# Kernel tuning notes

Hardware: AMD Instinct MI355X
Metric: run time of the kernel (lower is better)

The kernel has to match this reference:

```python
import jax, jax.numpy as jnp
import numpy as np

KSIZE, STRIDE, H, W = 7, 4, 128, 128
NH = (H - KSIZE) // STRIDE + 1  # 31
L = NH * NH                     # 961 patches


def conv2d(x, w, b=None, stride=1):
    y = jax.lax.conv_general_dilated(x, w, (stride, stride), 'VALID',
                                     dimension_numbers=('NCHW', 'OIHW', 'NCHW'))
    if b is not None:
        y = y + b[None, :, None, None]
    return y


def refpad(x):
    return jnp.pad(x, ((0, 0), (0, 0), (1, 1), (1, 1)), mode='reflect')


def unfold(x, k, s):
    # torch.nn.Unfold equivalent, returned as (B, C, k, k, L)
    B, C, Hh, Ww = x.shape
    nh = (Hh - k) // s + 1
    nw = (Ww - k) // s + 1
    hi = (jnp.arange(nh) * s)[:, None] + jnp.arange(k)  # (nh, k)
    wi = (jnp.arange(nw) * s)[:, None] + jnp.arange(k)  # (nw, k)
    p = x[:, :, hi]            # (B, C, nh, k, W)
    p = p[:, :, :, :, wi]      # (B, C, nh, k, nw, k)
    p = p.transpose(0, 1, 3, 5, 2, 4).reshape(B, C, k, k, nh * nw)
    return p


def fold(patches, Hh, Ww, k, s):
    # patches: (B, nh, nw, C, k, k); overlap-add like torch.nn.functional.fold
    B, nh, nw, C = patches.shape[0], patches.shape[1], patches.shape[2], patches.shape[3]
    hi = (jnp.arange(nh) * s)[:, None] + jnp.arange(k)  # (nh, k)
    wi = (jnp.arange(nw) * s)[:, None] + jnp.arange(k)  # (nw, k)
    H_idx = hi[:, None, :, None]  # (nh, 1, k, 1)
    W_idx = wi[None, :, None, :]  # (1, nw, 1, k)
    vals = patches.transpose(0, 3, 1, 2, 4, 5)  # (B, C, nh, nw, k, k)
    out = jnp.zeros((B, C, Hh, Ww), patches.dtype)
    return out.at[:, :, H_idx, W_idx].add(vals)


def setup_inputs() -> dict:
    key = jax.random.key(0)
    ks = jax.random.split(key, 16)
    Cin, Ci = 32, 16            # in_channels, inter_channels
    F_in = KSIZE * KSIZE * Ci   # 784
    F_out = F_in // 4           # 196
    s = 0.05
    d = {
        'x':       jax.random.normal(ks[0], (8, Cin, H, W), jnp.float32),
        'g_w':     jax.random.normal(ks[1], (Ci, Cin, 3, 3), jnp.float32) * s,
        'g_b':     jax.random.normal(ks[2], (Ci,), jnp.float32) * s,
        'w_w':     jax.random.normal(ks[3], (Ci, Cin, 3, 3), jnp.float32) * s,
        'w_b':     jax.random.normal(ks[4], (Ci,), jnp.float32) * s,
        'theta_w': jax.random.normal(ks[5], (Cin, Ci, 1, 1), jnp.float32) * s,
        'theta_b': jax.random.normal(ks[6], (Cin,), jnp.float32) * s,
        'fc1_w':   jax.random.normal(ks[7], (F_out, F_in), jnp.float32) * s,
        'fc1_b':   jax.random.normal(ks[8], (F_out,), jnp.float32) * s,
        'mconv_w': jax.random.normal(ks[9], (L, L), jnp.float32) * s,
        'mconv_b': jax.random.normal(ks[10], (L,), jnp.float32) * s,
        'mfc_w':   jax.random.normal(ks[11], (L, L), jnp.float32) * s,
        'mfc_b':   jax.random.normal(ks[12], (L,), jnp.float32) * s,
        'c1_w':    jax.random.normal(ks[13], (Cin // 2, Cin, 3, 3), jnp.float32) * s,
        'c2_w':    jax.random.normal(ks[14], (Cin, Cin // 2, 1, 1), jnp.float32) * s,
    }
    return d


def reference(x, g_w, g_b, w_w, w_b, theta_w, theta_b, fc1_w, fc1_b,
              mconv_w, mconv_b, mfc_w, mfc_b, c1_w, c2_w):
    residual = x
    x1 = conv2d(refpad(x), g_w, g_b)        # (B, Ci, H, W)
    x2 = conv2d(refpad(x), w_w, w_b)        # (B, Ci, H, W)
    x3 = conv2d(x1, theta_w, theta_b)       # (B, Cin, H, W)
    B = x.shape[0]
    Cin = x.shape[1]

    p6 = unfold(x1, KSIZE, STRIDE).transpose(0, 4, 1, 2, 3).reshape(B, L, -1)   # (B,L,Ci*49)
    p4 = unfold(x2, KSIZE, STRIDE).transpose(0, 4, 1, 2, 3).reshape(B, L, -1)   # (B,L,Ci*49)
    p62 = unfold(x3, KSIZE, STRIDE).transpose(0, 4, 1, 2, 3).reshape(B, L, -1)  # (B,L,Cin*49)

    wf = p4 @ fc1_w.T + fc1_b   # (B, L, F)
    xf = p6 @ fc1_w.T + fc1_b   # (B, L, F)
    A = jnp.einsum('blf,bmf->blm', wf, xf)  # (B, L, L)

    # Ti1 (Conv1d k=1 over patch dim) + Ti2 (Linear over patch dim, transposed)
    Ti = jnp.einsum('nc,bcm->bnm', mconv_w + mfc_w, A) + (mconv_b + mfc_b)[None, :, None]
    mask = jax.nn.sigmoid(Ti)
    mask_b = (mask != 0.0).astype(A.dtype)

    scale = wf.shape[-1] ** -0.5
    Am = jax.nn.softmax(A * mask * scale, axis=-1) * mask_b  # (B, L, L)

    y = jnp.einsum('blm,bmf->blf', Am, p62)  # (B, L, Cin*49)
    y = y.reshape(B, NH, NH, Cin, KSIZE, KSIZE)
    out = fold(y, H, W, KSIZE, STRIDE)       # (B, Cin, H, W)

    # BasicBlock: conv3x3(reflect) -> lrelu -> conv1x1 -> lrelu
    o = jax.nn.leaky_relu(conv2d(refpad(out), c1_w), 0.2)
    o = jax.nn.leaky_relu(conv2d(o, c2_w), 0.2)
    out = residual + o
    return Am, out
```

## Files before the change

kernel.cpp:

```cpp
#include <hip/hip_runtime.h>
#include <math.h>

namespace {
constexpr int Bn   = 8;
constexpr int CIN  = 32;
constexpr int CI   = 16;
constexpr int Lp   = 961;
constexpr int FIN  = 784;
constexpr int FOUT = 196;
constexpr int F62  = 1568;

constexpr int FCP  = 224;
constexpr long long FCB = 961LL * FCP;
constexpr int KP   = 992;
constexpr long long WFTB = 196LL * KP;
constexpr long long AMBB = 961LL * KP;
constexpr long long PBTB = 1568LL * KP;
constexpr long long AB   = 961LL * 961;
constexpr int YLD  = 964;
constexpr long long YB = 1568LL * YLD;
}

typedef __attribute__((ext_vector_type(8))) short short8x;
typedef __attribute__((ext_vector_type(4))) float floatx4;
typedef __attribute__((ext_vector_type(4))) unsigned short ushort4x;

static __device__ __forceinline__ unsigned short f2bf(float x) {
    unsigned int u = __builtin_bit_cast(unsigned int, x);
    u += 0x7fffu + ((u >> 16) & 1u);
    return (unsigned short)(u >> 16);
}
static __device__ __forceinline__ float bf2f(unsigned short h) {
    return __builtin_bit_cast(float, ((unsigned int)h) << 16);
}

__global__ __launch_bounds__(256)
void prep_k(const float* __restrict__ g_w, const float* __restrict__ w_w,
            const float* __restrict__ c1_w,
            float* __restrict__ wT1, float* __restrict__ wT2,
            float* __restrict__ wTc,
            const float* __restrict__ mconv_w, const float* __restrict__ mfc_w,
            unsigned short* __restrict__ Mwh, unsigned short* __restrict__ Mwl,
            const float* __restrict__ mconv_b, const float* __restrict__ mfc_b,
            float* __restrict__ Mb,
            const float* __restrict__ fc1w,
            unsigned short* __restrict__ Wh, unsigned short* __restrict__ Wl,
            unsigned short* __restrict__ wfTh, unsigned short* __restrict__ wfTl)
{
    int i = blockIdx.x * 256 + threadIdx.x;
    if (i < 13824) {
        int sel = i / 4608, r = i - sel * 4608;
        int tapidx = r >> 4, co = r & 15;
        const float* w = (sel == 0) ? g_w : (sel == 1) ? w_w : c1_w;
        float* t = (sel == 0) ? wT1 : (sel == 1) ? wT2 : wTc;
        t[r] = w[co * 288 + tapidx];
    } else if (i < 967136) {
        int k = i - 13824;
        int n = k / KP, c = k - n * KP;
        float v = (c < 961) ? (mconv_w[n * 961 + c] + mfc_w[n * 961 + c]) : 0.0f;
        unsigned short h = f2bf(v);
        Mwh[k] = h; Mwl[k] = f2bf(v - bf2f(h));
    } else if (i < 968097) {
        int k = i - 967136;
        Mb[k] = mconv_b[k] + mfc_b[k];
    } else if (i < 1172897) {
        int k = i - 968097;
        int n = k / 800, kk = k - n * 800;
        float v = (n < 196 && kk < 784) ? fc1w[n * 784 + kk] : 0.0f;
        unsigned short h = f2bf(v);
        Wh[k] = h; Wl[k] = f2bf(v - bf2f(h));
    } else if (i < 1223073) {
        int k = i - 1172897;
        int row = k >> 5, c = k & 31;
        long long pos = (long long)row * KP + 960 + c;
        wfTh[pos] = 0; wfTl[pos] = 0;
    }
}

template<bool DUAL, bool BIAS, bool LEAKY>
__global__ __launch_bounds__(256)
void conv3x3t_k(const float* __restrict__ x,
                const float* __restrict__ wT1, const float* __restrict__ b1,
                const float* __restrict__ wT2, const float* __restrict__ b2,
                float* __restrict__ o1, float* __restrict__ o2)
{
    __shared__ float Ls[10880];
    const int tid = threadIdx.x;
    const int t  = blockIdx.x;
    const int wt = t & 3, ht = (t >> 2) & 15, b = t >> 6;
    const int h0 = ht * 8, w0 = wt * 32;
    const float* xb = x + (size_t)b * CIN * 16384;

    for (int i = tid; i < 10880; i += 256) {
        int ci  = i / 340;
        int rem = i - ci * 340;
        int row = rem / 34;
        int col = rem - row * 34;
        int gh = h0 + row - 1; gh = (gh < 0) ? 1 : (gh > 127 ? 126 : gh);
        int gw = w0 + col - 1; gw = (gw < 0) ? 1 : (gw > 127 ? 126 : gw);
        Ls[i] = xb[ci * 16384 + gh * 128 + gw];
    }
    __syncthreads();

    const int px = tid & 31, py = tid >> 5;
    float acc1[16], acc2[16];
    #pragma unroll
    for (int co = 0; co < 16; ++co) {
        acc1[co] = BIAS ? b1[co] : 0.0f;
        acc2[co] = (DUAL && BIAS) ? b2[co] : 0.0f;
    }

    for (int ci = 0; ci < 32; ++ci) {
        const float* lp = &Ls[ci * 340 + py * 34 + px];
        float vv[9];
        #pragma unroll
        for (int r = 0; r < 3; ++r)
            #pragma unroll
            for (int c = 0; c < 3; ++c)
                vv[r * 3 + c] = lp[r * 34 + c];
        const float* wr1 = wT1 + ci * 144;
        const float* wr2 = DUAL ? (wT2 + ci * 144) : nullptr;
        #pragma unroll
        for (int tp = 0; tp < 9; ++tp) {
            float v = vv[tp];
            #pragma unroll
            for (int co = 0; co < 16; ++co) {
                acc1[co] += v * wr1[tp * 16 + co];
                if constexpr (DUAL) acc2[co] += v * wr2[tp * 16 + co];
            }
        }
    }

    const int h = h0 + py, w = w0 + px;
    size_t ob = (((size_t)b * 16) * 128 + h) * 128 + w;
    #pragma unroll
    for (int co = 0; co < 16; ++co) {
        float v = acc1[co];
        if constexpr (LEAKY) v = (v >= 0.0f) ? v : 0.2f * v;
        o1[ob + (size_t)co * 16384] = v;
        if constexpr (DUAL) o2[ob + (size_t)co * 16384] = acc2[co];
    }
}

template<bool BIAS, bool LEAKY, bool RESID>
__global__ __launch_bounds__(256)
void conv1x1p_k(const float* __restrict__ src, const float* __restrict__ wgt,
                const float* __restrict__ bias, const float* __restrict__ resid,
                float* __restrict__ out)
{
    int idx = blockIdx.x * 256 + threadIdx.x;
    int pix = idx & 16383;
    int b   = idx >> 14;
    const float* sb = src + (size_t)b * CI * 16384 + pix;
    float s[16];
    #pragma unroll
    for (int ci = 0; ci < CI; ++ci) s[ci] = sb[ci * 16384];
    size_t ob = (size_t)b * 32 * 16384 + pix;
    #pragma unroll
    for (int co = 0; co < 32; ++co) {
        const float* wrow = wgt + co * CI;
        float acc = BIAS ? bias[co] : 0.0f;
        #pragma unroll
        for (int ci = 0; ci < CI; ++ci) acc += wrow[ci] * s[ci];
        if constexpr (LEAKY) acc = (acc >= 0.0f) ? acc : 0.2f * acc;
        if constexpr (RESID) acc += resid[ob + (size_t)co * 16384];
        out[ob + (size_t)co * 16384] = acc;
    }
}

template<bool WRT>
__global__ __launch_bounds__(256)
void fcmfma_k(const float* __restrict__ xsrc,
              const unsigned short* __restrict__ Wh,
              const unsigned short* __restrict__ Wl,
              const float* __restrict__ bias,
              unsigned short* __restrict__ Dh, unsigned short* __restrict__ Dl,
              unsigned short* __restrict__ DTh, unsigned short* __restrict__ DTl)
{
    __shared__ unsigned short AsH[64*32], AsL[64*32], BsH[64*32], BsL[64*32];
    const int tid = threadIdx.x;
    const int tm0 = (blockIdx.x >> 2) * 64;
    const int tn0 = (blockIdx.x & 3) * 64;

    const int lr = tid >> 2;
    const int lc = tid & 3;
    const int gm = tm0 + lr;
    const bool mok = gm < 7688;
    int gbase = 0;
    if (mok) {
        int b = gm / 961, pi = gm - b * 961;
        int ih = pi / 31, iw = pi - ih * 31;
        gbase = b * 262144 + ih * 512 + iw * 4;
    }
    const int pc = ((lc ^ ((lr >> 1) & 3))) * 8;
    const unsigned short* Whr = Wh + (tn0 + lr) * 800;
    const unsigned short* Wlr = Wl + (tn0 + lr) * 800;

    const int lane = tid & 63, wv = tid >> 6;
    const int wm = (wv >> 1) * 32, wn = (wv & 1) * 32;
    const int fr = lane & 15, kq = lane >> 4;

    floatx4 acc[2][2];
    #pragma unroll
    for (int i = 0; i < 2; ++i)
        #pragma unroll
        for (int j = 0; j < 2; ++j)
            acc[i][j] = (floatx4){0.f, 0.f, 0.f, 0.f};

    float pv[8];
    short8x pwh, pwl;
    auto loadA = [&](int k0) {
        #pragma unroll
        for (int j = 0; j < 8; ++j) {
            int k = k0 + lc * 8 + j;
            float v = 0.0f;
            if (mok && k < 784) {
                int c  = k / 49, r = k - c * 49;
                int kh = r / 7,  kw = r - kh * 7;
                v = xsrc[gbase + c * 16384 + kh * 128 + kw];
            }
            pv[j] = v;
        }
    };
    auto loadW = [&](int k0) {
        pwh = *(const short8x*)(Whr + k0 + lc * 8);
        pwl = *(const short8x*)(Wlr + k0 + lc * 8);
    };

    loadA(0); loadW(0);
    for (int k0 = 0; k0 < 800; k0 += 32) {
        unsigned short hv[8], lv[8];
        #pragma unroll
        for (int j = 0; j < 8; ++j) {
            unsigned short h = f2bf(pv[j]);
            hv[j] = h; lv[j] = f2bf(pv[j] - bf2f(h));
        }
        *(short8x*)&AsH[lr * 32 + pc] = *(short8x*)hv;
        *(short8x*)&AsL[lr * 32 + pc] = *(short8x*)lv;
        *(short8x*)&BsH[lr * 32 + pc] = pwh;
        *(short8x*)&BsL[lr * 32 + pc] = pwl;
        __syncthreads();
        if (k0 + 32 < 800) { loadA(k0 + 32); loadW(k0 + 32); }
        short8x ah[2], al[2], bh[2], bl[2];
        #pragma unroll
        for (int i = 0; i < 2; ++i) {
            int mr = wm + i * 16 + fr;
            int off = mr * 32 + ((kq ^ ((mr >> 1) & 3)) * 8);
            ah[i] = *(const short8x*)&AsH[off];
            al[i] = *(const short8x*)&AsL[off];
        }
        #pragma unroll
        for (int j = 0; j < 2; ++j) {
            int nr = wn + j * 16 + fr;
            int off = nr * 32 + ((kq ^ ((nr >> 1) & 3)) * 8);
            bh[j] = *(const short8x*)&BsH[off];
            bl[j] = *(const short8x*)&BsL[off];
        }
        #pragma unroll
        for (int i = 0; i < 2; ++i)
            #pragma unroll
            for (int j = 0; j < 2; ++j) {
                acc[i][j] = __builtin_amdgcn_mfma_f32_16x16x32_bf16(ah[i], bh[j], acc[i][j], 0, 0, 0);
                acc[i][j] = __builtin_amdgcn_mfma_f32_16x16x32_bf16(ah[i], bl[j], acc[i][j], 0, 0, 0);
                acc[i][j] = __builtin_amdgcn_mfma_f32_16x16x32_bf16(al[i], bh[j], acc[i][j], 0, 0, 0);
            }
        __syncthreads();
    }

    #pragma unroll
    for (int j = 0; j < 2; ++j) {
        int n = tn0 + wn + j * 16 + fr;
        if (n >= FCP) continue;
        float bn = (n < 196) ? bias[n] : 0.0f;
        #pragma unroll
        for (int i = 0; i < 2; ++i) {
            #pragma unroll
            for (int r = 0; r < 4; ++r) {
                int l = tm0 + wm + i * 16 + kq * 4 + r;
                if (l >= 7688) continue;
                int b = l / 961, pi = l - b * 961;
                float v = (n < 196) ? (acc[i][j][r] + bn) : 0.0f;
                unsigned short h = f2bf(v);
                unsigned short lo = f2bf(v - bf2f(h));
                long long base = (long long)b * FCB + (long long)pi * FCP + n;
                Dh[base] = h;
                Dl[base] = lo;
                if constexpr (WRT) {
                    if (n < 196) {
                        long long tb = (long long)b * WFTB + (long long)n * KP + pi;
                        DTh[tb] = h;
                        DTl[tb] = lo;
                    }
                }
            }
        }
    }
}

__global__ __launch_bounds__(256)
void w2mfma_k(const unsigned short* __restrict__ Xhi,
              const unsigned short* __restrict__ Xlo,
              const unsigned short* __restrict__ Yhi,
              const unsigned short* __restrict__ Ylo,
              unsigned short* __restrict__ W2h,
              unsigned short* __restrict__ W2l)
{
    __shared__ unsigned short XsH[4096], XsL[4096], YsH[4096], YsL[4096];
    const int b   = blockIdx.x & 7;
    const int t   = blockIdx.x >> 3;
    const int tm0 = (t >> 1) * 128;
    const int tn0 = (t & 1) * 128;
    const unsigned short* Ybh = Yhi + (long long)b * WFTB;
    const unsigned short* Ybl = Ylo + (long long)b * WFTB;
    const int tid = threadIdx.x;

    const int sr  = tid >> 1;
    const int sc0 = (tid & 1) * 2;
    const bool xok = (tm0 + sr) < 961;
    const bool yok = (tn0 + sr) < 196;
    const unsigned short* Xrh = Xhi + (long long)(tm0 + sr) * KP;
    const unsigned short* Xrl = Xlo + (long long)(tm0 + sr) * KP;
    const unsigned short* Yrh = Ybh + (long long)(tn0 + sr) * KP;
    const unsigned short* Yrl = Ybl + (long long)(tn0 + sr) * KP;
    const int swz = (sr >> 1) & 3;

    const int lane = tid & 63;
    const int wv   = tid >> 6;
    const int wm   = (wv >> 1) * 64, wn = (wv & 1) * 64;
    const int fr   = lane & 15;
    const int kq   = lane >> 4;

    floatx4 acc[4][4];
    #pragma unroll
    for (int i = 0; i < 4; ++i)
        #pragma unroll
        for (int j = 0; j < 4; ++j)
            acc[i][j] = (floatx4){0.f, 0.f, 0.f, 0.f};

    const short8x zz = {0,0,0,0,0,0,0,0};
    short8x pxh[2], pxl[2], pyh[2], pyl[2];
    auto loadK = [&](int k0) {
        #pragma unroll
        for (int c = 0; c < 2; ++c) {
            int kc = sc0 + c;
            pxh[c] = xok ? *(const short8x*)(Xrh + k0 + kc * 8) : zz;
            pxl[c] = xok ? *(const short8x*)(Xrl + k0 + kc * 8) : zz;
            pyh[c] = yok ? *(const short8x*)(Yrh + k0 + kc * 8) : zz;
            pyl[c] = yok ? *(const short8x*)(Yrl + k0 + kc * 8) : zz;
        }
    };

    loadK(0);
    for (int k0 = 0; k0 < KP; k0 += 32) {
        #pragma unroll
        for (int c = 0; c < 2; ++c) {
            int pc = (sc0 + c) ^ swz;
            *(short8x*)&XsH[sr * 32 + pc * 8] = pxh[c];
            *(short8x*)&XsL[sr * 32 + pc * 8] = pxl[c];
            *(short8x*)&YsH[sr * 32 + pc * 8] = pyh[c];
            *(short8x*)&YsL[sr * 32 + pc * 8] = pyl[c];
        }
        __syncthreads();
        if (k0 + 32 < KP) loadK(k0 + 32);
        short8x bh[4], bl[4];
        #pragma unroll
        for (int j = 0; j < 4; ++j) {
            int nr = wn + j * 16 + fr;
            int off = nr * 32 + ((kq ^ ((nr >> 1) & 3)) * 8);
            bh[j] = *(const short8x*)&YsH[off];
            bl[j] = *(const short8x*)&YsL[off];
        }
        #pragma unroll
        for (int i = 0; i < 4; ++i) {
            int mr = wm + i * 16 + fr;
            int off = mr * 32 + ((kq ^ ((mr >> 1) & 3)) * 8);
            short8x ah = *(const short8x*)&XsH[off];
            short8x al = *(const short8x*)&XsL[off];
            #pragma unroll
            for (int j = 0; j < 4; ++j) {
                acc[i][j] = __builtin_amdgcn_mfma_f32_16x16x32_bf16(ah, bh[j], acc[i][j], 0, 0, 0);
                acc[i][j] = __builtin_amdgcn_mfma_f32_16x16x32_bf16(ah, bl[j], acc[i][j], 0, 0, 0);
                acc[i][j] = __builtin_amdgcn_mfma_f32_16x16x32_bf16(al, bh[j], acc[i][j], 0, 0, 0);
            }
        }
        __syncthreads();
    }

    unsigned short* Wh2 = W2h + (long long)b * FCB;
    unsigned short* Wl2 = W2l + (long long)b * FCB;
    #pragma unroll
    for (int j = 0; j < 4; ++j) {
        int f = tn0 + wn + j * 16 + fr;
        if (f >= FCP) continue;
        #pragma unroll
        for (int i = 0; i < 4; ++i) {
            int lb = tm0 + wm + i * 16 + kq * 4;
            #pragma unroll
            for (int r = 0; r < 4; ++r) {
                int l = lb + r;
                if (l >= 961) continue;
                float v = acc[i][j][r];
                unsigned short h = f2bf(v);
                long long pos = (long long)l * FCP + f;
                Wh2[pos] = h;
                Wl2[pos] = f2bf(v - bf2f(h));
            }
        }
    }
}

__global__ __launch_bounds__(256)
void atimfma_k(const unsigned short* __restrict__ Wfh,
               const unsigned short* __restrict__ Wfl,
               const unsigned short* __restrict__ W2h,
               const unsigned short* __restrict__ W2l,
               const unsigned short* __restrict__ Xfh,
               const unsigned short* __restrict__ Xfl,
               const float* __restrict__ Mb,
               float* __restrict__ Sout)
{
    __shared__ unsigned short smem[24576];
    unsigned short* X1H = smem;
    unsigned short* X1L = smem + 4096;
    unsigned short* X2H = smem + 8192;
    unsigned short* X2L = smem + 12288;
    unsigned short* YH  = smem + 16384;
    unsigned short* YL  = smem + 20480;

    const int b   = blockIdx.x & 7;
    const int t   = blockIdx.x >> 3;
    const int tm0 = (t >> 3) * 128;
    const int tn0 = (t & 7) * 128;
    const int tid = threadIdx.x;

    const int sr  = tid >> 1;
    const int sc0 = (tid & 1) * 2;
    const bool xok = (tm0 + sr) < 961;
    const bool yok = (tn0 + sr) < 961;
    const unsigned short* X1rh = Wfh + (long long)b * FCB + (long long)(tm0 + sr) * FCP;
    const unsigned short* X1rl = Wfl + (long long)b * FCB + (long long)(tm0 + sr) * FCP;
    const unsigned short* X2rh = W2h + (long long)b * FCB + (long long)(tm0 + sr) * FCP;
    const unsigned short* X2rl = W2l + (long long)b * FCB + (long long)(tm0 + sr) * FCP;
    const unsigned short* Yrh  = Xfh + (long long)b * FCB + (long long)(tn0 + sr) * FCP;
    const unsigned short* Yrl  = Xfl + (long long)b * FCB + (long long)(tn0 + sr) * FCP;
    const int swz = (sr >> 1) & 3;

    const int lane = tid & 63;
    const int wv   = tid >> 6;
    const int wm   = (wv >> 1) * 64, wn = (wv & 1) * 64;
    const int fr   = lane & 15;
    const int kq   = lane >> 4;

    floatx4 accA[4][4], accT[4][4];
    #pragma unroll
    for (int i = 0; i < 4; ++i)
        #pragma unroll
        for (int j = 0; j < 4; ++j) {
            accA[i][j] = (floatx4){0.f, 0.f, 0.f, 0.f};
            accT[i][j] = (floatx4){0.f, 0.f, 0.f, 0.f};
        }

    const short8x zz = {0,0,0,0,0,0,0,0};
    short8x p1h[2], p1l[2], p2h[2], p2l[2], pyh[2], pyl[2];
    auto loadK = [&](int k0) {
        #pragma unroll
        for (int c = 0; c < 2; ++c) {
            int kc = sc0 + c;
            p1h[c] = xok ? *(const short8x*)(X1rh + k0 + kc * 8) : zz;
            p1l[c] = xok ? *(const short8x*)(X1rl + k0 + kc * 8) : zz;
            p2h[c] = xok ? *(const short8x*)(X2rh + k0 + kc * 8) : zz;
            p2l[c] = xok ? *(const short8x*)(X2rl + k0 + kc * 8) : zz;
            pyh[c] = yok ? *(const short8x*)(Yrh  + k0 + kc * 8) : zz;
            pyl[c] = yok ? *(const short8x*)(Yrl  + k0 + kc * 8) : zz;
        }
    };

    loadK(0);
    for (int k0 = 0; k0 < FCP; k0 += 32) {
        #pragma unroll
        for (int c = 0; c < 2; ++c) {
            int pc = (sc0 + c) ^ swz;
            *(short8x*)&X1H[sr * 32 + pc * 8] = p1h[c];
            *(short8x*)&X1L[sr * 32 + pc * 8] = p1l[c];
            *(short8x*)&X2H[sr * 32 + pc * 8] = p2h[c];
            *(short8x*)&X2L[sr * 32 + pc * 8] = p2l[c];
            *(short8x*)&YH[sr * 32 + pc * 8]  = pyh[c];
            *(short8x*)&YL[sr * 32 + pc * 8]  = pyl[c];
        }
        __syncthreads();
        if (k0 + 32 < FCP) loadK(k0 + 32);
        short8x bh[4], bl[4];
        #pragma unroll
        for (int j = 0; j < 4; ++j) {
            int nr = wn + j * 16 + fr;
            int off = nr * 32 + ((kq ^ ((nr >> 1) & 3)) * 8);
            bh[j] = *(const short8x*)&YH[off];
            bl[j] = *(const short8x*)&YL[off];
        }
        #pragma unroll
        for (int i = 0; i < 4; ++i) {
            int mr = wm + i * 16 + fr;
            int off = mr * 32 + ((kq ^ ((mr >> 1) & 3)) * 8);
            short8x a1h = *(const short8x*)&X1H[off];
            short8x a1l = *(const short8x*)&X1L[off];
            short8x a2h = *(const short8x*)&X2H[off];
            short8x a2l = *(const short8x*)&X2L[off];
            #pragma unroll
            for (int j = 0; j < 4; ++j) {
                accA[i][j] = __builtin_amdgcn_mfma_f32_16x16x32_bf16(a1h, bh[j], accA[i][j], 0, 0, 0);
                accA[i][j] = __builtin_amdgcn_mfma_f32_16x16x32_bf16(a1h, bl[j], accA[i][j], 0, 0, 0);
                accA[i][j] = __builtin_amdgcn_mfma_f32_16x16x32_bf16(a1l, bh[j], accA[i][j], 0, 0, 0);
                accT[i][j] = __builtin_amdgcn_mfma_f32_16x16x32_bf16(a2h, bh[j], accT[i][j], 0, 0, 0);
                accT[i][j] = __builtin_amdgcn_mfma_f32_16x16x32_bf16(a2h, bl[j], accT[i][j], 0, 0, 0);
                accT[i][j] = __builtin_amdgcn_mfma_f32_16x16x32_bf16(a2l, bh[j], accT[i][j], 0, 0, 0);
            }
        }
        __syncthreads();
    }

    const float scale = 0.07142857142857142f;
    float* Sb = Sout + (long long)b * AB;
    #pragma unroll
    for (int j = 0; j < 4; ++j) {
        int m = tn0 + wn + j * 16 + fr;
        if (m >= 961) continue;
        #pragma unroll
        for (int i = 0; i < 4; ++i) {
            int lb = tm0 + wm + i * 16 + kq * 4;
            #pragma unroll
            for (int r = 0; r < 4; ++r) {
                int l = lb + r;
                if (l >= 961) continue;
                float ti = accT[i][j][r] + Mb[l];
                float mask = 1.0f / (1.0f + expf(-ti));
                Sb[(long long)l * 961 + m] = accA[i][j][r] * mask * scale;
            }
        }
    }
}

__global__ __launch_bounds__(256)
void softmax_mask_k(const float* __restrict__ S, float* __restrict__ Am,
                    unsigned short* __restrict__ Amb)
{
    int row = blockIdx.x;
    const float* srow = S + (long long)row * Lp;
    float*       orow = Am + (long long)row * Lp;
    unsigned short* brow = Amb + (long long)row * KP;
    int tid = threadIdx.x;

    float s[4], mb[4];
    float lmax = -INFINITY;
    #pragma unroll
    for (int j = 0; j < 4; ++j) {
        int m = tid + j * 256;
        if (m < Lp) {
            float v = srow[m];
            s[j]  = v;
            mb[j] = (v != 0.0f) ? 1.0f : 0.0f;
            lmax  = fmaxf(lmax, v);
        } else { s[j] = -INFINITY; mb[j] = 0.0f; }
    }
    __shared__ float red[256];
    red[tid] = lmax; __syncthreads();
    #pragma unroll
    for (int off = 128; off > 0; off >>= 1) {
        if (tid < off) red[tid] = fmaxf(red[tid], red[tid + off]);
        __syncthreads();
    }
    float rmax = red[0];
    __syncthreads();

    float e[4];
    float lsum = 0.0f;
    #pragma unroll
    for (int j = 0; j < 4; ++j) {
        int m = tid + j * 256;
        e[j] = (m < Lp) ? expf(s[j] - rmax) : 0.0f;
        lsum += e[j];
    }
    red[tid] = lsum; __syncthreads();
    #pragma unroll
    for (int off = 128; off > 0; off >>= 1) {
        if (tid < off) red[tid] += red[tid + off];
        __syncthreads();
    }
    float inv = 1.0f / red[0];
    #pragma unroll
    for (int j = 0; j < 4; ++j) {
        int m = tid + j * 256;
        if (m < Lp) {
            float v = e[j] * inv * mb[j];
            orow[m] = v;
            brow[m] = f2bf(v);
        } else if (m < KP) {
            brow[m] = 0;
        }
    }
}

__global__ __launch_bounds__(256)
void p62bt_k(const float* __restrict__ x3, unsigned short* __restrict__ out)
{
    int idx = blockIdx.x * 256 + threadIdx.x;
    if (idx >= 8 * 1568 * 124) return;
    int ck = idx % 124;
    int t  = idx / 124;
    int n  = t % 1568;
    int b  = t / 1568;
    int c = n / 49, rr = n - c * 49;
    int kh = rr / 7, kw = rr - kh * 7;
    const float* src = x3 + (long long)b * 524288 + c * 16384 + kh * 128 + kw;
    int k = ck * 8;
    unsigned short v[8];
    #pragma unroll
    for (int j = 0; j < 8; ++j) {
        int kk = k + j;
        if (kk < Lp) {
            int ih = kk / 31, iw = kk - ih * 31;
            v[j] = f2bf(src[ih * 512 + iw * 4]);
        } else v[j] = 0;
    }
    *(short8x*)(out + ((long long)b * 1568 + n) * KP + k) = *(short8x*)v;
}

__global__ __launch_bounds__(256)
void ymfma_k(const unsigned short* __restrict__ Amb,
             const unsigned short* __restrict__ Pbt,
             unsigned short* __restrict__ yT)
{
    __shared__ unsigned short As[128 * 32];
    __shared__ unsigned short Bs[128 * 32];
    const int b   = blockIdx.x & 7;
    const int t   = blockIdx.x >> 3;
    const int tn0 = (t % 13) * 128;
    const int tm0 = (t / 13) * 128;
    const unsigned short* Ab = Amb + (long long)b * AMBB;
    const unsigned short* Bb = Pbt + (long long)b * PBTB;
    const int tid = threadIdx.x;

    const int sr  = tid >> 1;
    const int sc0 = (tid & 1) * 2;
    const bool aok = (tm0 + sr) < Lp;
    const bool bok = (tn0 + sr) < F62;
    const unsigned short* Arow = Ab + (long long)(tm0 + sr) * KP;
    const unsigned short* Brow = Bb + (long long)(tn0 + sr) * KP;
    const int swz = (sr >> 1) & 3;

    const int lane = tid & 63;
    const int wv   = tid >> 6;
    const int wm   = (wv >> 1) * 64, wn = (wv & 1) * 64;
    const int fr   = lane & 15;
    const int kq   = lane >> 4;

    floatx4 acc[4][4];
    #pragma unroll
    for (int i = 0; i < 4; ++i)
        #pragma unroll
        for (int j = 0; j < 4; ++j)
            acc[i][j] = (floatx4){0.f, 0.f, 0.f, 0.f};

    const short8x zz = {0,0,0,0,0,0,0,0};
    short8x pa[2], pb[2];
    auto loadK = [&](int k0) {
        #pragma unroll
        for (int c = 0; c < 2; ++c) {
            int kc = sc0 + c;
            pa[c] = aok ? *(const short8x*)(Arow + k0 + kc * 8) : zz;
            pb[c] = bok ? *(const short8x*)(Brow + k0 + kc * 8) : zz;
        }
    };

    loadK(0);
    for (int k0 = 0; k0 < Lp; k0 += 32) {
        #pragma unroll
        for (int c = 0; c < 2; ++c) {
            int pc = (sc0 + c) ^ swz;
            *(short8x*)&As[sr * 32 + pc * 8] = pa[c];
            *(short8x*)&Bs[sr * 32 + pc * 8] = pb[c];
        }
        __syncthreads();
        if (k0 + 32 < Lp) loadK(k0 + 32);
        short8x af[4], bfr[4];
        #pragma unroll
        for (int i = 0; i < 4; ++i) {
            int mr = wm + i * 16 + fr;
            af[i] = *(const short8x*)&As[mr * 32 + ((kq ^ ((mr >> 1) & 3)) * 8)];
        }
        #pragma unroll
        for (int j = 0; j < 4; ++j) {
            int nr = wn + j * 16 + fr;
            bfr[j] = *(const short8x*)&Bs[nr * 32 + ((kq ^ ((nr >> 1) & 3)) * 8)];
        }
        #pragma unroll
        for (int i = 0; i < 4; ++i)
            #pragma unroll
            for (int j = 0; j < 4; ++j)
                acc[i][j] = __builtin_amdgcn_mfma_f32_16x16x32_bf16(
                                af[i], bfr[j], acc[i][j], 0, 0, 0);
        __syncthreads();
    }

    unsigned short* Yb = yT + (long long)b * YB;
    #pragma unroll
    for (int j = 0; j < 4; ++j) {
        int n = tn0 + wn + j * 16 + fr;
        if (n >= F62) continue;
        unsigned short* Yr = Yb + (long long)n * YLD;
        #pragma unroll
        for (int i = 0; i < 4; ++i) {
            int lb = tm0 + wm + i * 16 + kq * 4;
            if (lb >= Lp) continue;
            ushort4x hv;
            #pragma unroll
            for (int r = 0; r < 4; ++r) hv[r] = f2bf(acc[i][j][r]);
            if (lb + 3 < Lp) {
                *(ushort4x*)(Yr + lb) = hv;
            } else {
                #pragma unroll
                for (int r = 0; r < 4; ++r)
                    if (lb + r < Lp) Yr[lb + r] = hv[r];
            }
        }
    }
}

__global__ __launch_bounds__(256)
void foldg_k(const unsigned short* __restrict__ yT, float* __restrict__ out)
{
    int idx = blockIdx.x * 256 + threadIdx.x;
    int wc = idx & 127;
    int hr = (idx >> 7) & 127;
    int c  = (idx >> 14) & 31;
    int b  = idx >> 19;
    int ih_lo = (hr >= 6) ? ((hr - 3) >> 2) : 0;
    int ih_hi = min(hr >> 2, 30);
    int iw_lo = (wc >= 6) ? ((wc - 3) >> 2) : 0;
    int iw_hi = min(wc >> 2, 30);
    const unsigned short* Yb = yT + (long long)b * YB + (long long)c * 49 * YLD;
    float acc = 0.0f;
    for (int ih = ih_lo; ih <= ih_hi; ++ih) {
        int kh = hr - 4 * ih;
        for (int iw = iw_lo; iw <= iw_hi; ++iw) {
            int kw = wc - 4 * iw;
            acc += bf2f(Yb[(kh * 7 + kw) * YLD + ih * 31 + iw]);
        }
    }
    out[idx] = acc;
}

extern "C" void kernel_launch(void* const* d_in, const int* in_sizes, int n_in,
                              void* d_out, int out_size, void* d_ws, size_t ws_size,
                              hipStream_t stream)
{
    const float* x       = (const float*)d_in[0];
    const float* g_w     = (const float*)d_in[1];
    const float* g_b     = (const float*)d_in[2];
    const float* w_w     = (const float*)d_in[3];
    const float* w_b     = (const float*)d_in[4];
    const float* theta_w = (const float*)d_in[5];
    const float* theta_b = (const float*)d_in[6];
    const float* fc1_w   = (const float*)d_in[7];
    const float* fc1_b   = (const float*)d_in[8];
    const float* mconv_w = (const float*)d_in[9];
    const float* mconv_b = (const float*)d_in[10];
    const float* mfc_w   = (const float*)d_in[11];
    const float* mfc_b   = (const float*)d_in[12];
    const float* c1_w    = (const float*)d_in[13];
    const float* c2_w    = (const float*)d_in[14];

    float* Am_out    = (float*)d_out;
    float* final_out = Am_out + (size_t)Bn * Lp * Lp;

    float* ws = (float*)d_ws;
    float* x1    = ws;
    float* x2    = ws + 2097152;
    float* x3    = ws + 4194304;
    unsigned short* xf_hi = (unsigned short*)(ws + 8388608);
    unsigned short* xf_lo = (unsigned short*)(ws + 9249664);
    unsigned short* wf_hi = (unsigned short*)(ws + 10110720);
    unsigned short* wf_lo = (unsigned short*)(ws + 10971776);
    float* Abuf  = ws + 11832832;
    unsigned short* wfT_hi = (unsigned short*)(ws + 19221000);
    unsigned short* wfT_lo = (unsigned short*)(ws + 19998728);
    unsigned short* W2_hi  = (unsigned short*)(ws + 20776456);
    unsigned short* W2_lo  = (unsigned short*)(ws + 21637512);
    unsigned short* Mw_hi = (unsigned short*)(ws + 26847496);
    unsigned short* Mw_lo = (unsigned short*)(ws + 27324152);
    float* Mb    = ws + 27800808;
    unsigned short* fc1wh = (unsigned short*)(ws + 27801832);
    unsigned short* fc1wl = (unsigned short*)(ws + 27904232);
    float* wT1   = ws + 28006632;
    float* wT2   = ws + 28011240;
    float* wTc   = ws + 28015848;
    unsigned short* Am_bf16 = (unsigned short*)x1;
    unsigned short* p62bT   = (unsigned short*)Abuf;
    unsigned short* yT      = wfT_hi;

    prep_k<<<4778, 256, 0, stream>>>(
        g_w, w_w, c1_w, wT1, wT2, wTc,
        mconv_w, mfc_w, Mw_hi, Mw_lo,
        mconv_b, mfc_b, Mb, fc1_w, fc1wh, fc1wl,
        wfT_hi, wfT_lo);

    conv3x3t_k<true, true, false><<<512, 256, 0, stream>>>(
        x, wT1, g_b, wT2, w_b, x1, x2);

    conv1x1p_k<true, false, false><<<512, 256, 0, stream>>>(
        x1, theta_w, theta_b, nullptr, x3);

    fcmfma_k<false><<<484, 256, 0, stream>>>(
        x1, fc1wh, fc1wl, fc1_b, xf_hi, xf_lo, nullptr, nullptr);
    fcmfma_k<true><<<484, 256, 0, stream>>>(
        x2, fc1wh, fc1wl, fc1_b, wf_hi, wf_lo, wfT_hi, wfT_lo);

    w2mfma_k<<<128, 256, 0, stream>>>(
        Mw_hi, Mw_lo, wfT_hi, wfT_lo, W2_hi, W2_lo);

    atimfma_k<<<512, 256, 0, stream>>>(
        wf_hi, wf_lo, W2_hi, W2_lo, xf_hi, xf_lo, Mb, Abuf);

    softmax_mask_k<<<7688, 256, 0, stream>>>(Abuf, Am_out, Am_bf16);

    p62bt_k<<<6077, 256, 0, stream>>>(x3, p62bT);

    ymfma_k<<<832, 256, 0, stream>>>(Am_bf16, p62bT, yT);

    foldg_k<<<16384, 256, 0, stream>>>(yT, x3);

    conv3x3t_k<false, false, true><<<512, 256, 0, stream>>>(
        x3, wTc, nullptr, nullptr, nullptr, x1, nullptr);

    conv1x1p_k<false, true, true><<<512, 256, 0, stream>>>(
        x1, c2_w, nullptr, x, final_out);
}
```

Before: 543.4 us.

## Load MFMA fragments directly from global memory with register double buffering

The A/T score GEMM kernel no longer stages its split-bf16 operand tiles through shared memory with barriers. Each lane now loads its MFMA fragments straight from global memory (L2) into a two-deep register buffer, prefetching the next K slice while computing the current one. Out-of-range rows are clamped instead of zeroed, and launch bounds request 2 blocks per CU. This removes LDS traffic and __syncthreads, but adds redundant global loads across waves (each operand is read by two waves) and higher register pressure, with 48 short8x fragments plus 32 accumulators.

```diff
diff --git a/kernel.cpp b/kernel.cpp
--- a/kernel.cpp
+++ b/kernel.cpp
@@ -409,7 +409,7 @@
     }
 }
 
-__global__ __launch_bounds__(256)
+__global__ __launch_bounds__(256, 2)
 void atimfma_k(const unsigned short* __restrict__ Wfh,
                const unsigned short* __restrict__ Wfl,
                const unsigned short* __restrict__ W2h,
@@ -419,38 +419,38 @@
                const float* __restrict__ Mb,
                float* __restrict__ Sout)
 {
-    __shared__ unsigned short smem[24576];
-    unsigned short* X1H = smem;
-    unsigned short* X1L = smem + 4096;
-    unsigned short* X2H = smem + 8192;
-    unsigned short* X2L = smem + 12288;
-    unsigned short* YH  = smem + 16384;
-    unsigned short* YL  = smem + 20480;
-
     const int b   = blockIdx.x & 7;
     const int t   = blockIdx.x >> 3;
     const int tm0 = (t >> 3) * 128;
     const int tn0 = (t & 7) * 128;
     const int tid = threadIdx.x;
 
-    const int sr  = tid >> 1;
-    const int sc0 = (tid & 1) * 2;
-    const bool xok = (tm0 + sr) < 961;
-    const bool yok = (tn0 + sr) < 961;
-    const unsigned short* X1rh = Wfh + (long long)b * FCB + (long long)(tm0 + sr) * FCP;
-    const unsigned short* X1rl = Wfl + (long long)b * FCB + (long long)(tm0 + sr) * FCP;
-    const unsigned short* X2rh = W2h + (long long)b * FCB + (long long)(tm0 + sr) * FCP;
-    const unsigned short* X2rl = W2l + (long long)b * FCB + (long long)(tm0 + sr) * FCP;
-    const unsigned short* Yrh  = Xfh + (long long)b * FCB + (long long)(tn0 + sr) * FCP;
-    const unsigned short* Yrl  = Xfl + (long long)b * FCB + (long long)(tn0 + sr) * FCP;
-    const int swz = (sr >> 1) & 3;
-
     const int lane = tid & 63;
     const int wv   = tid >> 6;
     const int wm   = (wv >> 1) * 64, wn = (wv & 1) * 64;
     const int fr   = lane & 15;
     const int kq   = lane >> 4;
 
+    const long long bb = (long long)b * FCB;
+    const unsigned short* A1h = Wfh + bb;
+    const unsigned short* A1l = Wfl + bb;
+    const unsigned short* A2h = W2h + bb;
+    const unsigned short* A2l = W2l + bb;
+    const unsigned short* Byh = Xfh + bb;
+    const unsigned short* Byl = Xfl + bb;
+
+    int aoff[4], boff[4];
+    #pragma unroll
+    for (int i = 0; i < 4; ++i) {
+        int r = tm0 + wm + i * 16 + fr; if (r > 960) r = 960;
+        aoff[i] = r * FCP + kq * 8;
+    }
+    #pragma unroll
+    for (int j = 0; j < 4; ++j) {
+        int r = tn0 + wn + j * 16 + fr; if (r > 960) r = 960;
+        boff[j] = r * FCP + kq * 8;
+    }
+
     floatx4 accA[4][4], accT[4][4];
     #pragma unroll
     for (int i = 0; i < 4; ++i)
@@ -460,62 +460,51 @@
             accT[i][j] = (floatx4){0.f, 0.f, 0.f, 0.f};
         }
 
-    const short8x zz = {0,0,0,0,0,0,0,0};
-    short8x p1h[2], p1l[2], p2h[2], p2l[2], pyh[2], pyl[2];
-    auto loadK = [&](int k0) {
-        #pragma unroll
-        for (int c = 0; c < 2; ++c) {
-            int kc = sc0 + c;
-            p1h[c] = xok ? *(const short8x*)(X1rh + k0 + kc * 8) : zz;
-            p1l[c] = xok ? *(const short8x*)(X1rl + k0 + kc * 8) : zz;
-            p2h[c] = xok ? *(const short8x*)(X2rh + k0 + kc * 8) : zz;
-            p2l[c] = xok ? *(const short8x*)(X2rl + k0 + kc * 8) : zz;
-            pyh[c] = yok ? *(const short8x*)(Yrh  + k0 + kc * 8) : zz;
-            pyl[c] = yok ? *(const short8x*)(Yrl  + k0 + kc * 8) : zz;
-        }
-    };
-
-    loadK(0);
-    for (int k0 = 0; k0 < FCP; k0 += 32) {
-        #pragma unroll
-        for (int c = 0; c < 2; ++c) {
-            int pc = (sc0 + c) ^ swz;
-            *(short8x*)&X1H[sr * 32 + pc * 8] = p1h[c];
-            *(short8x*)&X1L[sr * 32 + pc * 8] = p1l[c];
-            *(short8x*)&X2H[sr * 32 + pc * 8] = p2h[c];
-            *(short8x*)&X2L[sr * 32 + pc * 8] = p2l[c];
-            *(short8x*)&YH[sr * 32 + pc * 8]  = pyh[c];
-            *(short8x*)&YL[sr * 32 + pc * 8]  = pyl[c];
-        }
-        __syncthreads();
-        if (k0 + 32 < FCP) loadK(k0 + 32);
-        short8x bh[4], bl[4];
-        #pragma unroll
-        for (int j = 0; j < 4; ++j) {
-            int nr = wn + j * 16 + fr;
-            int off = nr * 32 + ((kq ^ ((nr >> 1) & 3)) * 8);
-            bh[j] = *(const short8x*)&YH[off];
-            bl[j] = *(const short8x*)&YL[off];
+    short8x f1h[2][4], f1l[2][4], f2h[2][4], f2l[2][4], fbh[2][4], fbl[2][4];
+
+    #pragma unroll
+    for (int j = 0; j < 4; ++j) {
+        fbh[0][j] = *(const short8x*)(Byh + boff[j]);
+        fbl[0][j] = *(const short8x*)(Byl + boff[j]);
+    }
+    #pragma unroll
+    for (int i = 0; i < 4; ++i) {
+        f1h[0][i] = *(const short8x*)(A1h + aoff[i]);
+        f1l[0][i] = *(const short8x*)(A1l + aoff[i]);
+        f2h[0][i] = *(const short8x*)(A2h + aoff[i]);
+        f2l[0][i] = *(const short8x*)(A2l + aoff[i]);
+    }
+
+    #pragma unroll
+    for (int ks = 0; ks < 7; ++ks) {
+        const int cur = ks & 1, nxt = cur ^ 1;
+        if (ks < 6) {
+            const int k0 = (ks + 1) * 32;
+            #pragma unroll
+            for (int j = 0; j < 4; ++j) {
+                fbh[nxt][j] = *(const short8x*)(Byh + boff[j] + k0);
+                fbl[nxt][j] = *(const short8x*)(Byl + boff[j] + k0);
+            }
+            #pragma unroll
+            for (int i = 0; i < 4; ++i) {
+                f1h[nxt][i] = *(const short8x*)(A1h + aoff[i] + k0);
+                f1l[nxt][i] = *(const short8x*)(A1l + aoff[i] + k0);
+                f2h[nxt][i] = *(const short8x*)(A2h + aoff[i] + k0);
+                f2l[nxt][i] = *(const short8x*)(A2l + aoff[i] + k0);
+            }
         }
         #pragma unroll
         for (int i = 0; i < 4; ++i) {
-            int mr = wm + i * 16 + fr;
-            int off = mr * 32 + ((kq ^ ((mr >> 1) & 3)) * 8);
-            short8x a1h = *(const short8x*)&X1H[off];
-            short8x a1l = *(const short8x*)&X1L[off];
-            short8x a2h = *(const short8x*)&X2H[off];
-            short8x a2l = *(const short8x*)&X2L[off];
             #pragma unroll
             for (int j = 0; j < 4; ++j) {
-                accA[i][j] = __builtin_amdgcn_mfma_f32_16x16x32_bf16(a1h, bh[j], accA[i][j], 0, 0, 0);
-                accA[i][j] = __builtin_amdgcn_mfma_f32_16x16x32_bf16(a1h, bl[j], accA[i][j], 0, 0, 0);
-                accA[i][j] = __builtin_amdgcn_mfma_f32_16x16x32_bf16(a1l, bh[j], accA[i][j], 0, 0, 0);
-                accT[i][j] = __builtin_amdgcn_mfma_f32_16x16x32_bf16(a2h, bh[j], accT[i][j], 0, 0, 0);
-                accT[i][j] = __builtin_amdgcn_mfma_f32_16x16x32_bf16(a2h, bl[j], accT[i][j], 0, 0, 0);
-                accT[i][j] = __builtin_amdgcn_mfma_f32_16x16x32_bf16(a2l, bh[j], accT[i][j], 0, 0, 0);
-            }
-        }
-        __syncthreads();
+                accA[i][j] = __builtin_amdgcn_mfma_f32_16x16x32_bf16(f1h[cur][i], fbh[cur][j], accA[i][j], 0, 0, 0);
+                accA[i][j] = __builtin_amdgcn_mfma_f32_16x16x32_bf16(f1h[cur][i], fbl[cur][j], accA[i][j], 0, 0, 0);
+                accA[i][j] = __builtin_amdgcn_mfma_f32_16x16x32_bf16(f1l[cur][i], fbh[cur][j], accA[i][j], 0, 0, 0);
+                accT[i][j] = __builtin_amdgcn_mfma_f32_16x16x32_bf16(f2h[cur][i], fbh[cur][j], accT[i][j], 0, 0, 0);
+                accT[i][j] = __builtin_amdgcn_mfma_f32_16x16x32_bf16(f2h[cur][i], fbl[cur][j], accT[i][j], 0, 0, 0);
+                accT[i][j] = __builtin_amdgcn_mfma_f32_16x16x32_bf16(f2l[cur][i], fbh[cur][j], accT[i][j], 0, 0, 0);
+            }
+        }
     }
 
     const float scale = 0.07142857142857142f;
```

Measured after the change: 525.8 us. 3.2% less time.
